# Kernel tuning notes

Measured on AMD Instinct MI355X. Metric: run time of the kernel, lower is better.

## Reference

```python
import jax, jax.numpy as jnp
import numpy as np


def conv3d(x, w, b):
    # x: [B,C,T,H,W], w: [O,I,3,3,3], padding=1, stride=1
    y = jax.lax.conv_general_dilated(
        x, w, window_strides=(1, 1, 1), padding=((1, 1), (1, 1), (1, 1)),
        dimension_numbers=('NCDHW', 'OIDHW', 'NCDHW'))
    return y + b[None, :, None, None, None]


def deform_conv3d(x, offsets, w, b):
    # Deformable 3D conv, kernel 3, pad 1, stride 1, no modulation mask.
    # offsets: [B, 81, T, H, W] -> [B, 27, 3(t,h,w), T, H, W]
    B, Cin, T, H, W = x.shape
    nk = 27
    off = offsets.reshape(B, nk, 3, T, H, W)
    r = jnp.arange(3, dtype=x.dtype) - 1.0  # kernel taps {-1,0,1}
    kt, kh, kw = jnp.meshgrid(r, r, r, indexing='ij')
    koff = jnp.stack([kt.ravel(), kh.ravel(), kw.ravel()], axis=-1)  # [27,3]
    bt = jnp.arange(T, dtype=x.dtype)[:, None, None]
    bh = jnp.arange(H, dtype=x.dtype)[None, :, None]
    bw = jnp.arange(W, dtype=x.dtype)[None, None, :]
    base = jnp.stack(jnp.broadcast_arrays(bt, bh, bw), axis=0)  # [3,T,H,W]
    pos = base[None, None] + koff[None, :, :, None, None, None] + off  # [B,27,3,T,H,W]
    pt, ph, pw = pos[:, :, 0], pos[:, :, 1], pos[:, :, 2]
    ft, fh, fw = jnp.floor(pt), jnp.floor(ph), jnp.floor(pw)
    at, ah, aw = pt - ft, ph - fh, pw - fw
    it, ih, iw = ft.astype(jnp.int32), fh.astype(jnp.int32), fw.astype(jnp.int32)
    N = T * H * W
    xf = x.reshape(B, Cin, N)
    gather = jax.vmap(lambda xb, lb: xb[:, lb])  # ([Cin,N],[27,N])->[Cin,27,N]
    acc = jnp.zeros((B, Cin, nk, N), dtype=x.dtype)
    # trilinear interpolation: accumulate 8 corners, zero outside bounds
    for dt in (0, 1):
        tti = it + dt
        wt = (1.0 - at) if dt == 0 else at
        vt = (tti >= 0) & (tti < T)
        tc = jnp.clip(tti, 0, T - 1)
        for dh in (0, 1):
            hhi = ih + dh
            wh = (1.0 - ah) if dh == 0 else ah
            vh = (hhi >= 0) & (hhi < H)
            hc = jnp.clip(hhi, 0, H - 1)
            for dw in (0, 1):
                wwi = iw + dw
                ww = (1.0 - aw) if dw == 0 else aw
                vw = (wwi >= 0) & (wwi < W)
                wc = jnp.clip(wwi, 0, W - 1)
                wgt = (wt * wh * ww) * (vt & vh & vw).astype(x.dtype)  # [B,27,T,H,W]
                lin = (tc * H + hc) * W + wc  # [B,27,T,H,W]
                g = gather(xf, lin.reshape(B, nk, N))  # [B,Cin,27,N]
                acc = acc + wgt.reshape(B, 1, nk, N) * g
    out = jnp.einsum('oik,bikn->bon', w.reshape(w.shape[0], Cin, nk), acc)
    out = out + b[None, :, None]
    return out.reshape(B, w.shape[0], T, H, W)


def setup_inputs() -> dict:
    key = jax.random.key(0)
    ks = jax.random.split(key, 12)
    B, Cin, Cout, mdim = 1, 256, 256, 256
    T, H, W = 8, 24, 24

    def winit(k, shape):
        fan_in = int(np.prod(shape[1:]))
        return jax.random.normal(k, shape, jnp.float32) / np.float32(np.sqrt(fan_in))

    return {
        'x': jax.random.normal(ks[0], (B, Cin, T, H, W), jnp.float32),
        'l1_w': winit(ks[1], (mdim, Cin, 3, 3, 3)),
        'l1_b': jnp.zeros((mdim,), jnp.float32),
        'l2_w': winit(ks[2], (mdim, mdim, 3, 3, 3)),
        'l2_b': jnp.zeros((mdim,), jnp.float32),
        'l3_w': winit(ks[3], (mdim, mdim, 3, 3, 3)),
        'l3_b': jnp.zeros((mdim,), jnp.float32),
        'def_w': winit(ks[4], (81, mdim, 3, 3, 3)) * 0.1,  # keep offsets small
        'def_b': jnp.zeros((81,), jnp.float32),
        'c3d_w': winit(ks[5], (Cout, Cin, 3, 3, 3)),
        'c3d_b': jnp.zeros((Cout,), jnp.float32),
    }


def reference(x, l1_w, l1_b, l2_w, l2_b, l3_w, l3_b, def_w, def_b, c3d_w, c3d_b):
    h = jax.nn.relu(conv3d(x, l1_w, l1_b))
    h = jax.nn.relu(conv3d(h, l2_w, l2_b))
    h = jax.nn.relu(conv3d(h, l3_w, l3_b))
    offsets = conv3d(h, def_w, def_b)  # [B,81,T,H,W]
    return deform_conv3d(x, offsets, c3d_w, c3d_b)
```

## Files before the change

### kernel.cpp

```cpp
#include <hip/hip_runtime.h>

#define TT 8
#define HH 24
#define WW 24
#define NN 4608
#define CIN 256
#define N3 6760
#define KDIM 6912
#define BK 64
#define KTILES 108
#define NSPLIT 6
#define KT_PER 18

typedef short short8 __attribute__((ext_vector_type(8)));
typedef short short4v __attribute__((ext_vector_type(4)));
typedef float f32x4  __attribute__((ext_vector_type(4)));
typedef int   i32x4  __attribute__((ext_vector_type(4)));
typedef unsigned int u32x4 __attribute__((ext_vector_type(4)));

#define MFMA16 __builtin_amdgcn_mfma_f32_16x16x32_bf16

__device__ __forceinline__ short f2bf(float f) {
    unsigned u = __float_as_uint(f);
    unsigned r = u + 0x7fffu + ((u >> 16) & 1u);
    return (short)(r >> 16);
}

__device__ __forceinline__ int n3_of(int n) {
    int t = n / (HH * WW), r = n % (HH * WW), h = r / WW, w = r % WW;
    return ((t + 1) * 26 + (h + 1)) * 26 + (w + 1);
}

__device__ __forceinline__ void gload16(const void* gsrc, void* lds) {
    __builtin_amdgcn_global_load_lds(
        (const __attribute__((address_space(1))) void*)gsrc,
        (__attribute__((address_space(3))) void*)lds, 16, 0, 0);
}

__global__ __launch_bounds__(256) void transpose_k(const float* __restrict__ x,
                                                   short* __restrict__ xbf3) {
    __shared__ float T[64][65];
    const int lane = threadIdx.x & 63, wave = threadIdx.x >> 6;
    const int n0 = blockIdx.x * 64, ci0 = blockIdx.y * 64;
    #pragma unroll
    for (int j = 0; j < 16; ++j) {
        int ci_l = wave * 16 + j;
        T[ci_l][lane] = x[(size_t)(ci0 + ci_l) * NN + n0 + lane];
    }
    __syncthreads();
    #pragma unroll
    for (int j = 0; j < 16; ++j) {
        int n_l = wave * 16 + j;
        xbf3[(size_t)n3_of(n0 + n_l) * 256 + ci0 + lane] = f2bf(T[lane][n_l]);
    }
}

__global__ void repack_w_k(const float* __restrict__ w, short* __restrict__ dst, int Cout) {
    int o = blockIdx.x, ci = threadIdx.x;
    const int row = o & 127, y = o >> 7;
    #pragma unroll
    for (int k = 0; k < 27; ++k) {
        int K = k * 256 + ci;
        int kt = K >> 6, kk = K & 63;
        int slot = (kk >> 3) ^ (row & 7), e = kk & 7;
        size_t idx = ((size_t)(y * KTILES + kt)) * 8192 + row * 64 + slot * 8 + e;
        float v = (o < Cout) ? w[((size_t)o * CIN + ci) * 27 + k] : 0.f;
        dst[idx] = f2bf(v);
    }
}

__global__ __launch_bounds__(256) void sample_k(
    const short* __restrict__ xbf3, const float* __restrict__ offs,
    short* __restrict__ S)
{
    __shared__ char recs[64 * 64];
    const int k = blockIdx.y, n0 = blockIdx.x * 64;
    const int tid = threadIdx.x;

    if (tid < 64) {
        const int n = n0 + tid;
        const int t = n / (HH * WW), r = n % (HH * WW), h = r / WW, w2 = r % WW;
        const int ki = k / 9, kj = (k % 9) / 3, kl = k % 3;
        const float pt = (float)(t  + ki - 1) + offs[(size_t)(k * 3 + 0) * NN + n];
        const float ph = (float)(h  + kj - 1) + offs[(size_t)(k * 3 + 1) * NN + n];
        const float pw = (float)(w2 + kl - 1) + offs[(size_t)(k * 3 + 2) * NN + n];
        const float ft = floorf(pt), fh = floorf(ph), fw = floorf(pw);
        const float at = pt - ft, ah = ph - fh, aw = pw - fw;
        const int it = (int)ft, ih = (int)fh, iw = (int)fw;
        i32x4 idx[2]; f32x4 wgt[2];
        #pragma unroll
        for (int dt = 0; dt < 2; ++dt)
        #pragma unroll
        for (int dh = 0; dh < 2; ++dh)
        #pragma unroll
        for (int dw = 0; dw < 2; ++dw) {
            const int c = (dt * 2 + dh) * 2 + dw;
            const int ti = it + dt, hi = ih + dh, wi = iw + dw;
            const bool v = (ti >= 0) && (ti < TT) && (hi >= 0) && (hi < HH) && (wi >= 0) && (wi < WW);
            float wv = (dt ? at : 1.f - at) * (dh ? ah : 1.f - ah) * (dw ? aw : 1.f - aw);
            const int tc = min(max(ti, 0), TT - 1), hc = min(max(hi, 0), HH - 1), wc = min(max(wi, 0), WW - 1);
            const int r3 = ((tc + 1) * 26 + (hc + 1)) * 26 + (wc + 1);
            idx[c >> 2][c & 3] = r3 * 512;
            wgt[c >> 2][c & 3] = v ? wv : 0.f;
        }
        char* rec = &recs[tid * 64];
        *(i32x4*)(rec)      = idx[0];
        *(i32x4*)(rec + 16) = idx[1];
        *(f32x4*)(rec + 32) = wgt[0];
        *(f32x4*)(rec + 48) = wgt[1];
    }
    __syncthreads();

    const int lane = tid & 63, wave = tid >> 6;
    const int half = lane >> 5, lch = lane & 31;
    const char* xb = (const char*)xbf3 + lch * 16;
    short* Sk = S + (size_t)k * NN * 256 + lch * 8;

    for (int i = 0; i < 16; i += 4) {
        const int na = wave * 16 + i + half;
        const int nb = na + 2;
        const char* ra = &recs[na * 64];
        const char* rb = &recs[nb * 64];
        const i32x4 ia0 = *(const i32x4*)(ra);
        const i32x4 ia1 = *(const i32x4*)(ra + 16);
        const f32x4 wa0 = *(const f32x4*)(ra + 32);
        const f32x4 wa1 = *(const f32x4*)(ra + 48);
        const i32x4 ib0 = *(const i32x4*)(rb);
        const i32x4 ib1 = *(const i32x4*)(rb + 16);
        const f32x4 wb0 = *(const f32x4*)(rb + 32);
        const f32x4 wb1 = *(const f32x4*)(rb + 48);

        u32x4 ga[8], gb[8];
        #pragma unroll
        for (int c = 0; c < 4; ++c) {
            ga[c]     = *(const u32x4*)(xb + ia0[c]);
            ga[c + 4] = *(const u32x4*)(xb + ia1[c]);
            gb[c]     = *(const u32x4*)(xb + ib0[c]);
            gb[c + 4] = *(const u32x4*)(xb + ib1[c]);
        }

        float sa[8] = {}, sb[8] = {};
        #pragma unroll
        for (int c = 0; c < 8; ++c) {
            const float va = (c < 4) ? wa0[c & 3] : wa1[c & 3];
            const float vb = (c < 4) ? wb0[c & 3] : wb1[c & 3];
            #pragma unroll
            for (int j = 0; j < 4; ++j) {
                sa[2*j]   = fmaf(va, __uint_as_float(ga[c][j] << 16),         sa[2*j]);
                sa[2*j+1] = fmaf(va, __uint_as_float(ga[c][j] & 0xffff0000u), sa[2*j+1]);
                sb[2*j]   = fmaf(vb, __uint_as_float(gb[c][j] << 16),         sb[2*j]);
                sb[2*j+1] = fmaf(vb, __uint_as_float(gb[c][j] & 0xffff0000u), sb[2*j+1]);
            }
        }
        short8 oa, ob;
        #pragma unroll
        for (int m = 0; m < 8; ++m) { oa[m] = f2bf(sa[m]); ob[m] = f2bf(sb[m]); }
        *(short8*)(Sk + (size_t)(n0 + na) * 256) = oa;
        *(short8*)(Sk + (size_t)(n0 + nb) * 256) = ob;
    }
}

template<int CP>
__global__ __launch_bounds__(256, 3) void gemm_conv_sk(
    const short* __restrict__ src,
    const short* __restrict__ wrb_sw,
    float* __restrict__ P)
{
    __shared__ short Ap[8192];
    __shared__ short Bw[8192];
    const int tid = threadIdx.x;
    const int l = tid & 63, w = tid >> 6;
    const int n0 = blockIdx.x * 128, co0 = blockIdx.y * 128, split = blockIdx.z;
    const int wr = w >> 1, wc = w & 1;
    const int lm = l & 15, lq = l >> 4;
    const int rswz = (lm & 7) << 3;
    const int kt0 = split * KT_PER;

    const int colA = 8 * ((l & 7) ^ ((l >> 3) & 7));
    int r3[4];
    #pragma unroll
    for (int j = 0; j < 4; ++j)
        r3[j] = n3_of(n0 + w * 32 + j * 8 + (l >> 3));
    const short* bbase = wrb_sw + ((size_t)blockIdx.y * KTILES) * 8192 + (w * 4) * 512 + l * 8;

    f32x4 acc[4][4] = {};

    for (int i = 0; i < KT_PER; ++i) {
        const int kt = kt0 + i;
        const int k = kt >> 2, ci0 = (kt & 3) * 64;
        const int dt = k / 9 - 1, dh = (k % 9) / 3 - 1, dw = k % 3 - 1;
        const int d3 = (dt * 26 + dh) * 26 + dw;
        #pragma unroll
        for (int j = 0; j < 4; ++j)
            gload16(src + (size_t)(r3[j] + d3) * 256 + ci0 + colA, &Ap[(w * 4 + j) * 512]);
        const short* b = bbase + (size_t)kt * 8192;
        #pragma unroll
        for (int j = 0; j < 4; ++j)
            gload16(b + j * 512, &Bw[(w * 4 + j) * 512]);
        __syncthreads();
        #pragma unroll
        for (int ks = 0; ks < 2; ++ks) {
            const int c = (ks * 32 + lq * 8) ^ rswz;
            short8 a[4], bf[4];
            #pragma unroll
            for (int m = 0; m < 4; ++m)
                a[m] = *(const short8*)&Ap[(wr * 64 + m * 16 + lm) * 64 + c];
            #pragma unroll
            for (int nb = 0; nb < 4; ++nb)
                bf[nb] = *(const short8*)&Bw[(wc * 64 + nb * 16 + lm) * 64 + c];
            #pragma unroll
            for (int m = 0; m < 4; ++m)
            #pragma unroll
            for (int nb = 0; nb < 4; ++nb)
                acc[m][nb] = MFMA16(a[m], bf[nb], acc[m][nb], 0, 0, 0);
        }
        __syncthreads();
    }
    #pragma unroll
    for (int m = 0; m < 4; ++m)
    #pragma unroll
    for (int nb = 0; nb < 4; ++nb) {
        int co = co0 + wc * 64 + nb * 16 + lm;
        int n = n0 + wr * 64 + m * 16 + lq * 4;
        *(f32x4*)(P + ((size_t)split * CP + co) * NN + n) = acc[m][nb];
    }
}

__global__ __launch_bounds__(256, 3) void gemm_deform_sk(
    const short* __restrict__ S,
    const short* __restrict__ wrb_sw,
    float* __restrict__ P)
{
    __shared__ short Ap[8192];
    __shared__ short Bw[8192];
    const int tid = threadIdx.x;
    const int l = tid & 63, w = tid >> 6;
    const int n0 = blockIdx.x * 128, co0 = blockIdx.y * 128, split = blockIdx.z;
    const int wr = w >> 1, wc = w & 1;
    const int lm = l & 15, lq = l >> 4;
    const int rswz = (lm & 7) << 3;
    const int kt0 = split * KT_PER;

    const int colA = 8 * ((l & 7) ^ ((l >> 3) & 7));
    int rA[4];
    #pragma unroll
    for (int j = 0; j < 4; ++j)
        rA[j] = n0 + w * 32 + j * 8 + (l >> 3);
    const short* bbase = wrb_sw + ((size_t)blockIdx.y * KTILES) * 8192 + (w * 4) * 512 + l * 8;

    f32x4 acc[4][4] = {};

    for (int i = 0; i < KT_PER; ++i) {
        const int kt = kt0 + i;
        const int k = kt >> 2, ci0 = (kt & 3) * 64;
        #pragma unroll
        for (int j = 0; j < 4; ++j)
            gload16(S + ((size_t)k * NN + rA[j]) * 256 + ci0 + colA, &Ap[(w * 4 + j) * 512]);
        const short* b = bbase + (size_t)kt * 8192;
        #pragma unroll
        for (int j = 0; j < 4; ++j)
            gload16(b + j * 512, &Bw[(w * 4 + j) * 512]);
        __syncthreads();
        #pragma unroll
        for (int ks = 0; ks < 2; ++ks) {
            const int c = (ks * 32 + lq * 8) ^ rswz;
            short8 a[4], bf[4];
            #pragma unroll
            for (int m = 0; m < 4; ++m)
                a[m] = *(const short8*)&Ap[(wr * 64 + m * 16 + lm) * 64 + c];
            #pragma unroll
            for (int nb = 0; nb < 4; ++nb)
                bf[nb] = *(const short8*)&Bw[(wc * 64 + nb * 16 + lm) * 64 + c];
            #pragma unroll
            for (int m = 0; m < 4; ++m)
            #pragma unroll
            for (int nb = 0; nb < 4; ++nb)
                acc[m][nb] = MFMA16(a[m], bf[nb], acc[m][nb], 0, 0, 0);
        }
        __syncthreads();
    }
    #pragma unroll
    for (int m = 0; m < 4; ++m)
    #pragma unroll
    for (int nb = 0; nb < 4; ++nb) {
        int co = co0 + wc * 64 + nb * 16 + lm;
        int n = n0 + wr * 64 + m * 16 + lq * 4;
        *(f32x4*)(P + ((size_t)split * 256 + co) * NN + n) = acc[m][nb];
    }
}

template<bool RELU>
__global__ __launch_bounds__(256) void reduce_k(
    const float* __restrict__ P, const float* __restrict__ bias,
    float* __restrict__ dst, int Cout, int CP)
{
    int id = blockIdx.x * 256 + threadIdx.x;
    int total = Cout * (NN / 4);
    if (id >= total) return;
    int co = id / (NN / 4), n4 = id - co * (NN / 4);
    const float* p0 = P + ((size_t)co) * NN + n4 * 4;
    f32x4 v = *(const f32x4*)p0;
    #pragma unroll
    for (int s = 1; s < NSPLIT; ++s) {
        f32x4 u = *(const f32x4*)(p0 + (size_t)s * CP * NN);
        #pragma unroll
        for (int q = 0; q < 4; ++q) v[q] += u[q];
    }
    float bv = bias[co];
    #pragma unroll
    for (int q = 0; q < 4; ++q) {
        float f = v[q] + bv;
        if (RELU) f = fmaxf(f, 0.f);
        v[q] = f;
    }
    *(f32x4*)(dst + (size_t)co * NN + n4 * 4) = v;
}

__global__ __launch_bounds__(256) void reduce_bf3(
    const float* __restrict__ P, const float* __restrict__ bias,
    short* __restrict__ dst)
{
    __shared__ float T[64][65];
    const int lane = threadIdx.x & 63, wave = threadIdx.x >> 6;
    const int n0 = blockIdx.x * 64, co0 = blockIdx.y * 64;
    #pragma unroll
    for (int j = 0; j < 16; ++j) {
        int co_l = wave * 16 + j, co = co0 + co_l;
        const float* p0 = P + (size_t)co * NN + n0 + lane;
        float a = p0[0];
        #pragma unroll
        for (int s = 1; s < NSPLIT; ++s) a += p0[(size_t)s * 256 * NN];
        T[co_l][lane] = fmaxf(a + bias[co], 0.f);
    }
    __syncthreads();
    #pragma unroll
    for (int j = 0; j < 16; ++j) {
        int n_l = wave * 16 + j;
        dst[(size_t)n3_of(n0 + n_l) * 256 + co0 + lane] = f2bf(T[lane][n_l]);
    }
}

extern "C" void kernel_launch(void* const* d_in, const int* in_sizes, int n_in,
                              void* d_out, int out_size, void* d_ws, size_t ws_size,
                              hipStream_t stream)
{
    const float* x   = (const float*)d_in[0];
    const float* l1w = (const float*)d_in[1];
    const float* l1b = (const float*)d_in[2];
    const float* l2w = (const float*)d_in[3];
    const float* l2b = (const float*)d_in[4];
    const float* l3w = (const float*)d_in[5];
    const float* l3b = (const float*)d_in[6];
    const float* dfw = (const float*)d_in[7];
    const float* dfb = (const float*)d_in[8];
    const float* c3w = (const float*)d_in[9];
    const float* c3b = (const float*)d_in[10];
    float* out = (float*)d_out;

    char* base = (char*)d_ws;
    short* S    = (short*)base;
    short* h1b  = (short*)(base);
    short* h2b  = (short*)(base + 3461120);
    short* h3b  = (short*)(base + 6922240);
    short* wrb1 = (short*)(base + 10383360);
    short* wrb2 = (short*)(base + 13922304);
    short* wrb3 = (short*)(base + 17461248);
    short* wrbd = (short*)(base + 21000192);
    char* q = base + 63700992;
    short* xbf3 = (short*)q; q += 3461120;
    float* offs = (float*)q; q += 1492992;
    short* wrbc = (short*)q; q += 3538944;
    float* P    = (float*)q;

    hipMemsetAsync(xbf3, 0, (size_t)N3 * 256 * 2, stream);
    hipMemsetAsync(h1b,  0, (size_t)3 * N3 * 256 * 2, stream);

    transpose_k<<<dim3(72, 4), dim3(256), 0, stream>>>(x, xbf3);
    repack_w_k<<<dim3(256), dim3(256), 0, stream>>>(l1w, wrb1, 256);
    repack_w_k<<<dim3(256), dim3(256), 0, stream>>>(l2w, wrb2, 256);
    repack_w_k<<<dim3(256), dim3(256), 0, stream>>>(l3w, wrb3, 256);
    repack_w_k<<<dim3(256), dim3(256), 0, stream>>>(c3w, wrbc, 256);
    repack_w_k<<<dim3(128), dim3(256), 0, stream>>>(dfw, wrbd, 81);

    const dim3 blk(256);
    const int rg81 = (81 * (NN / 4) + 255) / 256;
    const int rg256 = (256 * (NN / 4) + 255) / 256;

    gemm_conv_sk<256><<<dim3(36, 2, NSPLIT), blk, 0, stream>>>(xbf3, wrb1, P);
    reduce_bf3       <<<dim3(72, 4),         blk, 0, stream>>>(P, l1b, h1b);
    gemm_conv_sk<256><<<dim3(36, 2, NSPLIT), blk, 0, stream>>>(h1b, wrb2, P);
    reduce_bf3       <<<dim3(72, 4),         blk, 0, stream>>>(P, l2b, h2b);
    gemm_conv_sk<256><<<dim3(36, 2, NSPLIT), blk, 0, stream>>>(h2b, wrb3, P);
    reduce_bf3       <<<dim3(72, 4),         blk, 0, stream>>>(P, l3b, h3b);
    gemm_conv_sk<128><<<dim3(36, 1, NSPLIT), blk, 0, stream>>>(h3b, wrbd, P);
    reduce_k<false>  <<<dim3(rg81),          blk, 0, stream>>>(P, dfb, offs, 81, 128);

    sample_k<<<dim3(72, 27), blk, 0, stream>>>(xbf3, offs, S);
    gemm_deform_sk<<<dim3(36, 2, NSPLIT), blk, 0, stream>>>(S, wrbc, P);
    reduce_k<false><<<dim3(rg256), blk, 0, stream>>>(P, c3b, out, 256, 256);
}
```

Baseline: 231.4 us.

## Fuse split-K reduction into GEMM via last-block atomic counter; merge weight repacks

Each split-K GEMM block now increments a per-tile atomic counter after writing its partial sums, and the last block to arrive sums all splits, adds bias (and ReLU plus bf16 padded-layout transpose through LDS for the hidden layers), and writes the final output. This removes five separate reduction kernel launches and their extra pass over the partial buffer. The five weight repack launches are also merged into one 2D-grid launch. In exchange it adds an extra memset for the counters and serialized tail work in the last-arriving block, which depends on correct acquire/release ordering across blocks.

```diff
diff --git a/kernel.cpp b/kernel.cpp
--- a/kernel.cpp
+++ b/kernel.cpp
@@ -13,7 +13,6 @@
 #define KT_PER 18
 
 typedef short short8 __attribute__((ext_vector_type(8)));
-typedef short short4v __attribute__((ext_vector_type(4)));
 typedef float f32x4  __attribute__((ext_vector_type(4)));
 typedef int   i32x4  __attribute__((ext_vector_type(4)));
 typedef unsigned int u32x4 __attribute__((ext_vector_type(4)));
@@ -55,8 +54,19 @@
     }
 }
 
-__global__ void repack_w_k(const float* __restrict__ w, short* __restrict__ dst, int Cout) {
-    int o = blockIdx.x, ci = threadIdx.x;
+__global__ void repack_all_k(const float* __restrict__ w1, const float* __restrict__ w2,
+                             const float* __restrict__ w3, const float* __restrict__ wc,
+                             const float* __restrict__ wd,
+                             short* __restrict__ d1, short* __restrict__ d2,
+                             short* __restrict__ d3, short* __restrict__ dc,
+                             short* __restrict__ dd) {
+    const int sel = blockIdx.y, o = blockIdx.x, ci = threadIdx.x;
+    const float* w; short* dst; int Cout = 256;
+    if      (sel == 0) { w = w1; dst = d1; }
+    else if (sel == 1) { w = w2; dst = d2; }
+    else if (sel == 2) { w = w3; dst = d3; }
+    else if (sel == 3) { w = wc; dst = dc; }
+    else               { w = wd; dst = dd; Cout = 81; if (o >= 128) return; }
     const int row = o & 127, y = o >> 7;
     #pragma unroll
     for (int k = 0; k < 27; ++k) {
@@ -160,14 +170,17 @@
     }
 }
 
-template<int CP>
+template<int CP, bool BF3>
 __global__ __launch_bounds__(256, 3) void gemm_conv_sk(
     const short* __restrict__ src,
     const short* __restrict__ wrb_sw,
-    float* __restrict__ P)
+    float* __restrict__ P, int* __restrict__ cnt,
+    const float* __restrict__ bias, void* __restrict__ dstv, int Cout)
 {
-    __shared__ short Ap[8192];
-    __shared__ short Bw[8192];
+    __shared__ short ldsbuf[16384];
+    __shared__ int isLast;
+    short* Ap = ldsbuf;
+    short* Bw = ldsbuf + 8192;
     const int tid = threadIdx.x;
     const int l = tid & 63, w = tid >> 6;
     const int n0 = blockIdx.x * 128, co0 = blockIdx.y * 128, split = blockIdx.z;
@@ -216,6 +229,7 @@
         }
         __syncthreads();
     }
+
     #pragma unroll
     for (int m = 0; m < 4; ++m)
     #pragma unroll
@@ -224,15 +238,94 @@
         int n = n0 + wr * 64 + m * 16 + lq * 4;
         *(f32x4*)(P + ((size_t)split * CP + co) * NN + n) = acc[m][nb];
     }
+    __syncthreads();
+    if (tid == 0) {
+        int old = __hip_atomic_fetch_add(&cnt[blockIdx.y * gridDim.x + blockIdx.x], 1,
+                                         __ATOMIC_ACQ_REL, __HIP_MEMORY_SCOPE_AGENT);
+        isLast = (old == NSPLIT - 1);
+    }
+    __syncthreads();
+    if (!isLast) return;
+    __threadfence();
+
+    if (BF3) {
+        short* dst = (short*)dstv;
+        float* scratch = (float*)ldsbuf;
+        #pragma unroll
+        for (int q = 0; q < 4; ++q) {
+            if ((q >> 1) == wr && (q & 1) == wc) {
+                #pragma unroll
+                for (int nb = 0; nb < 4; ++nb) {
+                    int co = co0 + wc * 64 + nb * 16 + lm;
+                    float bv = bias[co];
+                    #pragma unroll
+                    for (int m = 0; m < 4; ++m) {
+                        int n = n0 + wr * 64 + m * 16 + lq * 4;
+                        f32x4 v = {};
+                        #pragma unroll
+                        for (int s = 0; s < NSPLIT; ++s) {
+                            f32x4 u = *(const f32x4*)(P + ((size_t)s * CP + co) * NN + n);
+                            #pragma unroll
+                            for (int j = 0; j < 4; ++j) v[j] += u[j];
+                        }
+                        #pragma unroll
+                        for (int j = 0; j < 4; ++j)
+                            scratch[(nb * 16 + lm) * 65 + m * 16 + lq * 4 + j] =
+                                fmaxf(v[j] + bv, 0.f);
+                    }
+                }
+            }
+            __syncthreads();
+            {
+                int n_l = tid >> 2, cq = (tid & 3) * 16;
+                int gn = n0 + (q >> 1) * 64 + n_l;
+                short8 o0, o1;
+                #pragma unroll
+                for (int j = 0; j < 8; ++j) o0[j] = f2bf(scratch[(cq + j) * 65 + n_l]);
+                #pragma unroll
+                for (int j = 0; j < 8; ++j) o1[j] = f2bf(scratch[(cq + 8 + j) * 65 + n_l]);
+                short* d = dst + (size_t)n3_of(gn) * 256 + co0 + (q & 1) * 64 + cq;
+                *(short8*)d = o0;
+                *(short8*)(d + 8) = o1;
+            }
+            __syncthreads();
+        }
+    } else {
+        float* dst = (float*)dstv;
+        #pragma unroll
+        for (int nb = 0; nb < 4; ++nb) {
+            int co = co0 + wc * 64 + nb * 16 + lm;
+            if (co < Cout) {
+                float bv = bias[co];
+                #pragma unroll
+                for (int m = 0; m < 4; ++m) {
+                    int n = n0 + wr * 64 + m * 16 + lq * 4;
+                    f32x4 v = {};
+                    #pragma unroll
+                    for (int s = 0; s < NSPLIT; ++s) {
+                        f32x4 u = *(const f32x4*)(P + ((size_t)s * CP + co) * NN + n);
+                        #pragma unroll
+                        for (int j = 0; j < 4; ++j) v[j] += u[j];
+                    }
+                    #pragma unroll
+                    for (int j = 0; j < 4; ++j) v[j] += bv;
+                    *(f32x4*)(dst + (size_t)co * NN + n) = v;
+                }
+            }
+        }
+    }
 }
 
 __global__ __launch_bounds__(256, 3) void gemm_deform_sk(
     const short* __restrict__ S,
     const short* __restrict__ wrb_sw,
-    float* __restrict__ P)
+    float* __restrict__ P, int* __restrict__ cnt,
+    const float* __restrict__ bias, float* __restrict__ dst)
 {
-    __shared__ short Ap[8192];
-    __shared__ short Bw[8192];
+    __shared__ short ldsbuf[16384];
+    __shared__ int isLast;
+    short* Ap = ldsbuf;
+    short* Bw = ldsbuf + 8192;
     const int tid = threadIdx.x;
     const int l = tid & 63, w = tid >> 6;
     const int n0 = blockIdx.x * 128, co0 = blockIdx.y * 128, split = blockIdx.z;
@@ -279,6 +372,7 @@
         }
         __syncthreads();
     }
+
     #pragma unroll
     for (int m = 0; m < 4; ++m)
     #pragma unroll
@@ -287,56 +381,34 @@
         int n = n0 + wr * 64 + m * 16 + lq * 4;
         *(f32x4*)(P + ((size_t)split * 256 + co) * NN + n) = acc[m][nb];
     }
-}
-
-template<bool RELU>
-__global__ __launch_bounds__(256) void reduce_k(
-    const float* __restrict__ P, const float* __restrict__ bias,
-    float* __restrict__ dst, int Cout, int CP)
-{
-    int id = blockIdx.x * 256 + threadIdx.x;
-    int total = Cout * (NN / 4);
-    if (id >= total) return;
-    int co = id / (NN / 4), n4 = id - co * (NN / 4);
-    const float* p0 = P + ((size_t)co) * NN + n4 * 4;
-    f32x4 v = *(const f32x4*)p0;
-    #pragma unroll
-    for (int s = 1; s < NSPLIT; ++s) {
-        f32x4 u = *(const f32x4*)(p0 + (size_t)s * CP * NN);
-        #pragma unroll
-        for (int q = 0; q < 4; ++q) v[q] += u[q];
-    }
-    float bv = bias[co];
-    #pragma unroll
-    for (int q = 0; q < 4; ++q) {
-        float f = v[q] + bv;
-        if (RELU) f = fmaxf(f, 0.f);
-        v[q] = f;
-    }
-    *(f32x4*)(dst + (size_t)co * NN + n4 * 4) = v;
-}
-
-__global__ __launch_bounds__(256) void reduce_bf3(
-    const float* __restrict__ P, const float* __restrict__ bias,
-    short* __restrict__ dst)
-{
-    __shared__ float T[64][65];
-    const int lane = threadIdx.x & 63, wave = threadIdx.x >> 6;
-    const int n0 = blockIdx.x * 64, co0 = blockIdx.y * 64;
-    #pragma unroll
-    for (int j = 0; j < 16; ++j) {
-        int co_l = wave * 16 + j, co = co0 + co_l;
-        const float* p0 = P + (size_t)co * NN + n0 + lane;
-        float a = p0[0];
-        #pragma unroll
-        for (int s = 1; s < NSPLIT; ++s) a += p0[(size_t)s * 256 * NN];
-        T[co_l][lane] = fmaxf(a + bias[co], 0.f);
-    }
-    __syncthreads();
-    #pragma unroll
-    for (int j = 0; j < 16; ++j) {
-        int n_l = wave * 16 + j;
-        dst[(size_t)n3_of(n0 + n_l) * 256 + co0 + lane] = f2bf(T[lane][n_l]);
+    __syncthreads();
+    if (tid == 0) {
+        int old = __hip_atomic_fetch_add(&cnt[blockIdx.y * gridDim.x + blockIdx.x], 1,
+                                         __ATOMIC_ACQ_REL, __HIP_MEMORY_SCOPE_AGENT);
+        isLast = (old == NSPLIT - 1);
+    }
+    __syncthreads();
+    if (!isLast) return;
+    __threadfence();
+
+    #pragma unroll
+    for (int nb = 0; nb < 4; ++nb) {
+        int co = co0 + wc * 64 + nb * 16 + lm;
+        float bv = bias[co];
+        #pragma unroll
+        for (int m = 0; m < 4; ++m) {
+            int n = n0 + wr * 64 + m * 16 + lq * 4;
+            f32x4 v = {};
+            #pragma unroll
+            for (int s = 0; s < NSPLIT; ++s) {
+                f32x4 u = *(const f32x4*)(P + ((size_t)s * 256 + co) * NN + n);
+                #pragma unroll
+                for (int j = 0; j < 4; ++j) v[j] += u[j];
+            }
+            #pragma unroll
+            for (int j = 0; j < 4; ++j) v[j] += bv;
+            *(f32x4*)(dst + (size_t)co * NN + n) = v;
+        }
     }
 }
 
@@ -370,32 +442,28 @@
     short* xbf3 = (short*)q; q += 3461120;
     float* offs = (float*)q; q += 1492992;
     short* wrbc = (short*)q; q += 3538944;
-    float* P    = (float*)q;
+    float* P    = (float*)q; q += (size_t)NSPLIT * 256 * NN * 4;
+    int*   cnt  = (int*)q;
 
     hipMemsetAsync(xbf3, 0, (size_t)N3 * 256 * 2, stream);
     hipMemsetAsync(h1b,  0, (size_t)3 * N3 * 256 * 2, stream);
+    hipMemsetAsync(cnt,  0, 5 * 128 * 4, stream);
 
     transpose_k<<<dim3(72, 4), dim3(256), 0, stream>>>(x, xbf3);
-    repack_w_k<<<dim3(256), dim3(256), 0, stream>>>(l1w, wrb1, 256);
-    repack_w_k<<<dim3(256), dim3(256), 0, stream>>>(l2w, wrb2, 256);
-    repack_w_k<<<dim3(256), dim3(256), 0, stream>>>(l3w, wrb3, 256);
-    repack_w_k<<<dim3(256), dim3(256), 0, stream>>>(c3w, wrbc, 256);
-    repack_w_k<<<dim3(128), dim3(256), 0, stream>>>(dfw, wrbd, 81);
+    repack_all_k<<<dim3(256, 5), dim3(256), 0, stream>>>(l1w, l2w, l3w, c3w, dfw,
+                                                         wrb1, wrb2, wrb3, wrbc, wrbd);
 
     const dim3 blk(256);
-    const int rg81 = (81 * (NN / 4) + 255) / 256;
-    const int rg256 = (256 * (NN / 4) + 255) / 256;
-
-    gemm_conv_sk<256><<<dim3(36, 2, NSPLIT), blk, 0, stream>>>(xbf3, wrb1, P);
-    reduce_bf3       <<<dim3(72, 4),         blk, 0, stream>>>(P, l1b, h1b);
-    gemm_conv_sk<256><<<dim3(36, 2, NSPLIT), blk, 0, stream>>>(h1b, wrb2, P);
-    reduce_bf3       <<<dim3(72, 4),         blk, 0, stream>>>(P, l2b, h2b);
-    gemm_conv_sk<256><<<dim3(36, 2, NSPLIT), blk, 0, stream>>>(h2b, wrb3, P);
-    reduce_bf3       <<<dim3(72, 4),         blk, 0, stream>>>(P, l3b, h3b);
-    gemm_conv_sk<128><<<dim3(36, 1, NSPLIT), blk, 0, stream>>>(h3b, wrbd, P);
-    reduce_k<false>  <<<dim3(rg81),          blk, 0, stream>>>(P, dfb, offs, 81, 128);
+    gemm_conv_sk<256, true ><<<dim3(36, 2, NSPLIT), blk, 0, stream>>>(
+        xbf3, wrb1, P, cnt + 0 * 128, l1b, h1b, 256);
+    gemm_conv_sk<256, true ><<<dim3(36, 2, NSPLIT), blk, 0, stream>>>(
+        h1b, wrb2, P, cnt + 1 * 128, l2b, h2b, 256);
+    gemm_conv_sk<256, true ><<<dim3(36, 2, NSPLIT), blk, 0, stream>>>(
+        h2b, wrb3, P, cnt + 2 * 128, l3b, h3b, 256);
+    gemm_conv_sk<128, false><<<dim3(36, 1, NSPLIT), blk, 0, stream>>>(
+        h3b, wrbd, P, cnt + 3 * 128, dfb, offs, 81);
 
     sample_k<<<dim3(72, 27), blk, 0, stream>>>(xbf3, offs, S);
-    gemm_deform_sk<<<dim3(36, 2, NSPLIT), blk, 0, stream>>>(S, wrbc, P);
-    reduce_k<false><<<dim3(rg256), blk, 0, stream>>>(P, c3b, out, 256, 256);
-}
+    gemm_deform_sk<<<dim3(36, 2, NSPLIT), blk, 0, stream>>>(
+        S, wrbc, P, cnt + 4 * 128, c3b, out);
+}
```

New measurement: 371.4 us. +60.5%, slower.
